# Kernel optimization log

Hardware: AMD Instinct MI355X
Metric: run time of the kernel (lower is better)

Reference implementation:

```python
import jax, jax.numpy as jnp
import numpy as np

B, T, L, D, H = 4, 8, 197, 512, 8
DK = D // H
SIM_TH = 0.0
N = T * (L - 1)  # 1568 local tokens

def _ln(x, g, b, eps=1e-5):
    x32 = x.astype(jnp.float32)
    m = jnp.mean(x32, axis=-1, keepdims=True)
    v = jnp.mean((x32 - m) ** 2, axis=-1, keepdims=True)
    return (((x32 - m) * jax.lax.rsqrt(v + eps)) * g + b).astype(x.dtype)

def _qgelu(x):
    return x * jax.nn.sigmoid(1.702 * x)

def _mha(x, w_in, b_in, w_out, b_out):
    # torch nn.MultiheadAttention, x: [S, Bt, D] (seq-first)
    S, Bt, _ = x.shape
    qkv = x @ w_in.T + b_in
    q, k, v = jnp.split(qkv, 3, axis=-1)
    q = q.reshape(S, Bt, H, DK); k = k.reshape(S, Bt, H, DK); v = v.reshape(S, Bt, H, DK)
    scores = jnp.einsum('sbhd,tbhd->bhst', q, k) / jnp.sqrt(jnp.asarray(DK, x.dtype))
    p = jax.nn.softmax(scores, axis=-1)
    o = jnp.einsum('bhst,tbhd->sbhd', p, v).reshape(S, Bt, D)
    return o @ w_out.T + b_out

def _resblock(x, ln1g, ln1b, inw, inb, outw, outb, ln2g, ln2b, fcw, fcb, pw, pb):
    x = x + _mha(_ln(x, ln1g, ln1b), inw, inb, outw, outb)
    h = _qgelu(_ln(x, ln2g, ln2b) @ fcw.T + fcb)
    return x + h @ pw.T + pb

def _build_graph(x, g_mask):
    xd = jax.lax.stop_gradient(x)  # matches x.detach()
    xn = xd / jnp.maximum(jnp.linalg.norm(xd, axis=-1, keepdims=True), 1e-12)
    sim = jnp.einsum('bnd,bmd->bnm', xn, xn)
    adj = jnp.where(sim < SIM_TH, 0.0, sim)
    return adj * g_mask  # t != 1 branch

def _graph_attn(x, mask, wq, bq, wk, bk, wv, bv, wo, bo):
    Bb, Nn, _ = x.shape
    def heads(a):
        return a.reshape(Bb, Nn, H, DK).transpose(0, 2, 1, 3)
    Q = heads(x @ wq.T + bq); K = heads(x @ wk.T + bk); V = heads(x @ wv.T + bv)
    scores = jnp.einsum('bhnd,bhmd->bhnm', Q, K) / jnp.sqrt(jnp.asarray(DK, x.dtype))
    m = mask[:, None]  # [b,1,N,N]
    scores = jnp.where(m == 0, -jnp.inf, scores * m)  # scores*mask then masked_fill(mask==0,-inf)
    p = jax.nn.softmax(scores, axis=-1)
    o = jnp.einsum('bhnm,bhmd->bhnd', p, V).transpose(0, 2, 1, 3).reshape(Bb, Nn, D)
    return o @ wo.T + bo

def _forward(x, proj_w, proj_b,
             m_ln1g, m_ln1b, m_inw, m_inb, m_outw, m_outb,
             m_ln2g, m_ln2b, m_fcw, m_fcb, m_pw, m_pb,
             g_wq, g_bq, g_wk, g_bk, g_wv, g_bv, g_wo, g_bo,
             ln1g, ln1b, a_inw, a_inb, a_outw, a_outb,
             ln2g, ln2b, fcw, fcb, pw, pb, g_mask):
    b, t, l, d = x.shape
    x = x @ proj_w.T + proj_b
    glob = x[:, :, 0, :].transpose(1, 0, 2)  # [t,b,d]
    msg = (m_ln1g, m_ln1b, m_inw, m_inb, m_outw, m_outb, m_ln2g, m_ln2b, m_fcw, m_fcb, m_pw, m_pb)
    glob = _resblock(glob, *msg)
    glob = _resblock(glob, *msg)  # message_attn applied twice (shared weights)
    glob = glob.reshape(1, t, b, d)
    loc = x[:, :, 1:, :].reshape(b, t * (l - 1), d)
    gm = _build_graph(loc, g_mask)
    loc = _graph_attn(loc, gm, g_wq, g_bq, g_wk, g_bk, g_wv, g_bv, g_wo, g_bo)
    loc = loc.reshape(b, t, l - 1, d).transpose(2, 1, 0, 3)  # [l-1,t,b,d]
    y = jnp.concatenate([glob, loc], axis=0).reshape(l, t * b, d)
    y = y + _mha(_ln(y, ln1g, ln1b), a_inw, a_inb, a_outw, a_outb)
    y = y + _qgelu(_ln(y, ln2g, ln2b) @ fcw.T + fcb) @ pw.T + pb
    return y.reshape(l, t, b, d).transpose(2, 1, 0, 3)  # [b,t,l,d]

def setup_inputs() -> dict:
    key = jax.random.key(0)
    ks = jax.random.split(key, 64)
    s = 0.02
    def w(i, shape):
        return jax.random.normal(ks[i], shape, jnp.float32) * s
    ones = jnp.ones((D,), jnp.float32); zeros = jnp.zeros((D,), jnp.float32)
    gm = (jax.random.uniform(ks[60], (N, N)) < 0.5).astype(jnp.float32)
    gm = gm.at[jnp.arange(N), jnp.arange(N)].set(1.0)  # keep self-edges so no row is fully masked
    return dict(
        x=jax.random.normal(ks[0], (B, T, L, D), jnp.float32),
        proj_w=w(1, (D, D)), proj_b=jnp.zeros((D,), jnp.float32),
        m_ln1g=ones, m_ln1b=zeros,
        m_inw=w(2, (3 * D, D)), m_inb=jnp.zeros((3 * D,), jnp.float32),
        m_outw=w(3, (D, D)), m_outb=zeros,
        m_ln2g=ones, m_ln2b=zeros,
        m_fcw=w(4, (4 * D, D)), m_fcb=jnp.zeros((4 * D,), jnp.float32),
        m_pw=w(5, (D, 4 * D)), m_pb=zeros,
        g_wq=w(6, (D, D)), g_bq=zeros, g_wk=w(7, (D, D)), g_bk=zeros,
        g_wv=w(8, (D, D)), g_bv=zeros, g_wo=w(9, (D, D)), g_bo=zeros,
        ln1g=ones, ln1b=zeros,
        a_inw=w(10, (3 * D, D)), a_inb=jnp.zeros((3 * D,), jnp.float32),
        a_outw=w(11, (D, D)), a_outb=zeros,
        ln2g=ones, ln2b=zeros,
        fcw=w(12, (4 * D, D)), fcb=jnp.zeros((4 * D,), jnp.float32),
        pw=w(13, (D, 4 * D)), pb=zeros,
        g_mask=gm,
    )

def reference(x, proj_w, proj_b, m_ln1g, m_ln1b, m_inw, m_inb, m_outw, m_outb,
              m_ln2g, m_ln2b, m_fcw, m_fcb, m_pw, m_pb,
              g_wq, g_bq, g_wk, g_bk, g_wv, g_bv, g_wo, g_bo,
              ln1g, ln1b, a_inw, a_inb, a_outw, a_outb,
              ln2g, ln2b, fcw, fcb, pw, pb, g_mask):
    return _forward(x, proj_w, proj_b, m_ln1g, m_ln1b, m_inw, m_inb, m_outw, m_outb,
                    m_ln2g, m_ln2b, m_fcw, m_fcb, m_pw, m_pb,
                    g_wq, g_bq, g_wk, g_bk, g_wv, g_bv, g_wo, g_bo,
                    ln1g, ln1b, a_inw, a_inb, a_outw, a_outb,
                    ln2g, ln2b, fcw, fcb, pw, pb, g_mask)
```

## Files before the change

### kernel.cpp

```cpp
#include <hip/hip_runtime.h>
#include <hip/hip_bf16.h>

typedef unsigned short u16;
typedef __attribute__((ext_vector_type(8))) short bf16x8;
typedef __attribute__((ext_vector_type(4))) float f32x4;

#define FINF __builtin_huge_valf()

static __device__ __forceinline__ float bf2f(u16 v){ union{unsigned u; float f;} c; c.u = ((unsigned)v)<<16; return c.f; }
static __device__ __forceinline__ u16 f2bf(float f){ union{__hip_bfloat16 h; u16 u;} c; c.h = __float2bfloat16(f); return c.u; }
static __device__ __forceinline__ bf16x8 scale8(bf16x8 v, float s){
  bf16x8 o;
  #pragma unroll
  for (int e=0;e<8;e++) o[e] = (short)f2bf(bf2f((u16)v[e])*s);
  return o;
}

static __device__ __forceinline__ void gload16(const void* g, void* l){
  __builtin_amdgcn_global_load_lds(
      (const __attribute__((address_space(1))) void*)g,
      (__attribute__((address_space(3))) void*)l, 16, 0, 0);
}

#define WAIT_VM0()   { asm volatile("s_waitcnt vmcnt(0)" ::: "memory"); __builtin_amdgcn_sched_barrier(0); }
#define BARRIER()    { __builtin_amdgcn_sched_barrier(0); __builtin_amdgcn_s_barrier(); __builtin_amdgcn_sched_barrier(0); }

struct CvtArgs {
  const float* src[14];
  u16* dst[14];
  int n[14];
};
__global__ __launch_bounds__(256) void cvt_multi(CvtArgs a){
  int seg = blockIdx.y;
  const float* s = a.src[seg]; u16* d = a.dst[seg]; int n = a.n[seg];
  for (int i = (blockIdx.x*256 + threadIdx.x)*4; i < n; i += gridDim.x*256*4){
    float4 v = *(const float4*)(s + i);
    ushort4 o = { f2bf(v.x), f2bf(v.y), f2bf(v.z), f2bf(v.w) };
    *(ushort4*)(d + i) = o;
  }
}

__global__ __launch_bounds__(256) void concat_bias(const float* a, const float* b, const float* c, float* o){
  int i = blockIdx.x*256 + threadIdx.x;
  o[i] = i < 512 ? a[i] : (i < 1024 ? b[i-512] : c[i-1024]);
}

template<int BM, int EPI>
__global__ __launch_bounds__(256,2) void gemm_nt(
    const u16* __restrict__ A, const u16* __restrict__ Bw,
    const float* __restrict__ bias, const float* aux, void* out,
    int M, int Nn, int K, int ldc, long aBatch, long bBatch, long cBatch)
{
  constexpr int MI = BM/32;
  constexpr int WSPAN = BM/2;
  __shared__ __align__(16) u16 a_lds[2*BM*64];
  __shared__ __align__(16) u16 b_lds[2*128*64];
  const int z = blockIdx.z;
  const u16* Az = A + (long)z*aBatch;
  const u16* Bz = Bw + (long)z*bBatch;
  const int n0 = blockIdx.x*128, m0 = blockIdx.y*BM;
  const int t = threadIdx.x, lane = t & 63, wave = t >> 6;
  const int wr = wave >> 1, wc = wave & 1;
  const int r = lane & 15, kq = lane >> 4;

  const int srow = t >> 3;
  const int scol = ((t&7)*8) ^ ((srow&7)<<3);
  int rowA[MI], rowB[4];
  #pragma unroll
  for (int i=0;i<MI;i++){ int ga = m0 + i*32 + srow; rowA[i] = ga < M ? ga : M-1; }
  #pragma unroll
  for (int i=0;i<4;i++){ int gb = n0 + i*32 + srow; rowB[i] = gb < Nn ? gb : Nn-1; }

  f32x4 acc[MI][4] = {};
  const int nkt = K >> 6;

  auto STAGE = [&](int kt, int buf){
    const long koff = (long)kt*64 + scol;
    #pragma unroll
    for (int i=0;i<MI;i++)
      gload16(Az + (long)rowA[i]*K + koff, (char*)a_lds + buf*(BM*128) + i*4096 + wave*1024);
    #pragma unroll
    for (int i=0;i<4;i++)
      gload16(Bz + (long)rowB[i]*K + koff, (char*)b_lds + buf*16384 + i*4096 + wave*1024);
  };

  STAGE(0,0);
  WAIT_VM0(); BARRIER();
  for (int kt=0; kt<nkt; kt++){
    const int cur = kt&1;
    if (kt+1 < nkt) STAGE(kt+1, cur^1);
    const u16* al = a_lds + cur*BM*64;
    const u16* bl = b_lds + cur*8192;
    #pragma unroll
    for (int kk=0; kk<2; kk++){
      bf16x8 af[MI], bfr[4];
      #pragma unroll
      for (int i=0;i<MI;i++){
        int rw = wr*WSPAN + i*16 + r;
        af[i] = *(const bf16x8*)&al[rw*64 + ((kk*32 + kq*8) ^ ((rw&7)<<3))];
      }
      #pragma unroll
      for (int j=0;j<4;j++){
        int rw = wc*64 + j*16 + r;
        bfr[j] = *(const bf16x8*)&bl[rw*64 + ((kk*32 + kq*8) ^ ((rw&7)<<3))];
      }
      #pragma unroll
      for (int i=0;i<MI;i++)
        #pragma unroll
        for (int j=0;j<4;j++)
          acc[i][j] = __builtin_amdgcn_mfma_f32_16x16x32_bf16(af[i], bfr[j], acc[i][j], 0,0,0);
    }
    WAIT_VM0(); BARRIER();
  }

  #pragma unroll
  for (int i=0;i<MI;i++){
    #pragma unroll
    for (int j=0;j<4;j++){
      int gcol = n0 + wc*64 + j*16 + r;
      if (gcol >= Nn) continue;
      float bv = bias ? bias[gcol] : 0.f;
      #pragma unroll
      for (int rr=0; rr<4; rr++){
        int grow = m0 + wr*WSPAN + i*16 + kq*4 + rr;
        if (grow >= M) continue;
        float v = acc[i][j][rr] + bv;
        if constexpr (EPI==0){
          ((float*)out)[(long)z*cBatch + (long)grow*ldc + gcol] = v;
        } else if constexpr (EPI==1){
          ((u16*)out)[(long)z*cBatch + (long)grow*ldc + gcol] = f2bf(v);
        } else if constexpr (EPI==2){
          long idx = (long)z*cBatch + (long)grow*ldc + gcol;
          ((float*)out)[idx] = aux[idx] + v;
        } else if constexpr (EPI==3){
          float g = v / (1.f + __expf(-1.702f*v));
          ((u16*)out)[(long)z*cBatch + (long)grow*ldc + gcol] = f2bf(g);
        } else if constexpr (EPI==4){
          float adj = v < 0.f ? 0.f : v;
          float gmv = aux[(long)grow*Nn + gcol];
          ((u16*)out)[(long)z*cBatch + (long)grow*ldc + gcol] = f2bf(adj*gmv);
        } else if constexpr (EPI==5){
          int b = grow/1568, n = grow%1568, tt = n/196, lp = n%196;
          int yrow = (1+lp)*32 + tt*4 + b;
          ((float*)out)[(long)yrow*ldc + gcol] = v;
        } else if constexpr (EPI==6){
          long idx = (long)grow*ldc + gcol;
          int l = grow>>5, rb = grow&31, tt = rb>>2, bb = rb&3;
          ((float*)out)[((long)((bb*8+tt)*197) + l)*512 + gcol] = aux[idx] + v;
        }
      }
    }
  }
}

template<bool MASKED>
__global__ __launch_bounds__(512,4) void flash_attn(
    const u16* __restrict__ QKV, const u16* __restrict__ gmask, u16* __restrict__ Out,
    int nq, int nk, long qBatch, long qRow, long oBatch, long oRow, long gmBatch)
{
  __shared__ __align__(16) u16 k_lds[2*4096];
  __shared__ __align__(16) u16 vt[64*72];
  __shared__ __align__(16) u16 p_lds[8][16*72];
  __shared__ __align__(16) u16 g_lds[MASKED ? 2*8192 : 8];
  const int t = threadIdx.x, lane = t&63, wave = t>>6;
  const int r = lane&15, kq = lane>>4;
  const int h = blockIdx.y, z = blockIdx.z;
  const u16* Qb = QKV + (long)z*qBatch + h*64;
  const u16* Kb = Qb + 512;
  const u16* Vb = Qb + 1024;
  const u16* Gz = gmask + (long)z*gmBatch;
  const int qt0 = blockIdx.x*128;
  const int q0  = qt0 + wave*16;

  bf16x8 qf0, qf1;
  { int qi = q0 + r; if (qi > nq-1) qi = nq-1;
    const u16* qp = Qb + (long)qi*qRow + kq*8;
    qf0 = scale8(*(const bf16x8*)qp, 0.125f);
    qf1 = scale8(*(const bf16x8*)(qp+32), 0.125f); }

  const int srow = t>>3;
  const int scol = ((t&7)*8) ^ ((srow&7)<<3);
  const int vcc  = (t&7)*8;

  uint4 vv;
  auto stage_k = [&](int kt, int buf){
    int j = kt*64 + srow; if (j > nk-1) j = nk-1;
    gload16(Kb + (long)j*qRow + scol, (char*)k_lds + buf*8192 + wave*1024);
  };
  auto stage_g = [&](int kt, int buf){
    #pragma unroll
    for (int i=0;i<2;i++){
      int qr = qt0 + i*64 + srow; if (qr > nq-1) qr = nq-1;
      gload16(Gz + (long)qr*nk + kt*64 + scol, (char*)g_lds + buf*16384 + i*8192 + wave*1024);
    }
  };
  auto load_v = [&](int kt){
    int vj = kt*64 + srow; if (vj > nk-1) vj = nk-1;
    vv = *(const uint4*)(Vb + (long)vj*qRow + vcc);
  };
  auto write_vt = [&](){
    #pragma unroll
    for (int e=0;e<8;e++)
      vt[(vcc+e)*72 + (srow ^ (e<<3))] = ((const u16*)&vv)[e];
  };

  bf16x8 ONES;
  #pragma unroll
  for (int e=0;e<8;e++) ONES[e] = (short)0x3F80;

  float m_[4] = {-FINF,-FINF,-FINF,-FINF};
  f32x4 o_[4] = {}; f32x4 ol = {};

  const int nkt = (nk + 63) >> 6;
  stage_k(0,0); if (MASKED) stage_g(0,0); load_v(0);
  __syncthreads();
  for (int kt=0; kt<nkt; kt++){
    const int cur = kt&1;
    write_vt();
    __syncthreads();
    if (kt+1 < nkt){
      stage_k(kt+1, cur^1);
      if (MASKED) stage_g(kt+1, cur^1);
      load_v(kt+1);
    }

    float s[4][4];
    const u16* kl = k_lds + cur*4096;
    #pragma unroll
    for (int sub=0; sub<4; sub++){
      int rw = sub*16 + r; int sw = (rw&7)<<3;
      bf16x8 kf0 = *(const bf16x8*)&kl[rw*64 + ((kq*8) ^ sw)];
      bf16x8 kf1 = *(const bf16x8*)&kl[rw*64 + ((32 + kq*8) ^ sw)];
      f32x4 sc = {};
      sc = __builtin_amdgcn_mfma_f32_16x16x32_bf16(qf0, kf0, sc, 0,0,0);
      sc = __builtin_amdgcn_mfma_f32_16x16x32_bf16(qf1, kf1, sc, 0,0,0);
      #pragma unroll
      for (int rr=0;rr<4;rr++) s[sub][rr] = sc[rr];
    }
    #pragma unroll
    for (int sub=0; sub<4; sub++){
      int key = kt*64 + sub*16 + r;
      bool kdead = key >= nk;
      #pragma unroll
      for (int rr=0;rr<4;rr++){
        float sv = s[sub][rr];
        if constexpr (MASKED){
          int lrow = wave*16 + kq*4 + rr;
          u16 g = g_lds[cur*8192 + lrow*64 + ((sub*16+r) ^ ((lrow&7)<<3))];
          if (g == 0 || kdead) sv = -FINF; else sv *= bf2f(g);
        } else {
          if (kdead) sv = -FINF;
        }
        s[sub][rr] = sv;
      }
    }
    #pragma unroll
    for (int rr=0;rr<4;rr++){
      float mx = fmaxf(fmaxf(s[0][rr],s[1][rr]), fmaxf(s[2][rr],s[3][rr]));
      #pragma unroll
      for (int d=1; d<16; d<<=1) mx = fmaxf(mx, __shfl_xor(mx, d));
      float mnew = fmaxf(m_[rr], mx);
      float fac = (m_[rr] == -FINF) ? 0.f : __expf(m_[rr] - mnew);
      #pragma unroll
      for (int sub=0;sub<4;sub++)
        s[sub][rr] = (s[sub][rr] == -FINF) ? 0.f : __expf(s[sub][rr] - mnew);
      m_[rr] = mnew;
      o_[0][rr]*=fac; o_[1][rr]*=fac; o_[2][rr]*=fac; o_[3][rr]*=fac; ol[rr]*=fac;
    }
    #pragma unroll
    for (int rr=0;rr<4;rr++){
      int prow = kq*4+rr;
      #pragma unroll
      for (int sub=0;sub<4;sub++)
        p_lds[wave][prow*72 + ((sub*16+r) ^ ((prow&7)<<3))] = f2bf(s[sub][rr]);
    }
    #pragma unroll
    for (int c=0;c<2;c++){
      bf16x8 pf = *(const bf16x8*)&p_lds[wave][r*72 + ((c*32 + kq*8) ^ ((r&7)<<3))];
      #pragma unroll
      for (int j=0;j<4;j++){
        bf16x8 vf = *(const bf16x8*)&vt[(j*16+r)*72 + ((c*32 + kq*8) ^ ((r&7)<<3))];
        o_[j] = __builtin_amdgcn_mfma_f32_16x16x32_bf16(pf, vf, o_[j], 0,0,0);
      }
      ol = __builtin_amdgcn_mfma_f32_16x16x32_bf16(pf, ONES, ol, 0,0,0);
    }
    __syncthreads();
  }

  #pragma unroll
  for (int rr=0;rr<4;rr++){
    int qrow = q0 + kq*4 + rr;
    if (qrow >= nq) continue;
    float inv = ol[rr] > 0.f ? 1.f/ol[rr] : 0.f;
    #pragma unroll
    for (int j=0;j<4;j++)
      Out[(long)z*oBatch + (long)qrow*oRow + h*64 + j*16 + r] = f2bf(o_[j][rr]*inv);
  }
}

__global__ __launch_bounds__(256) void ln_rows(const float* __restrict__ in,
    const float* __restrict__ g, const float* __restrict__ b, u16* __restrict__ out, int rows)
{
  int wave = threadIdx.x >> 6, lane = threadIdx.x & 63;
  int row = blockIdx.x*4 + wave;
  if (row >= rows) return;
  const float4* x = (const float4*)(in + (long)row*512);
  float4 v0 = x[lane], v1 = x[lane+64];
  float s  = v0.x+v0.y+v0.z+v0.w + v1.x+v1.y+v1.z+v1.w;
  float ss = v0.x*v0.x+v0.y*v0.y+v0.z*v0.z+v0.w*v0.w + v1.x*v1.x+v1.y*v1.y+v1.z*v1.z+v1.w*v1.w;
  #pragma unroll
  for (int d=1; d<64; d<<=1){ s += __shfl_xor(s,d); ss += __shfl_xor(ss,d); }
  float mean = s * (1.f/512.f);
  float var = ss * (1.f/512.f) - mean*mean;
  float rs = rsqrtf(var + 1e-5f);
  const float4* gg = (const float4*)g; const float4* bb = (const float4*)b;
  float4 g0 = gg[lane], g1 = gg[lane+64], b0 = bb[lane], b1 = bb[lane+64];
  u16* o = out + (long)row*512;
  ushort4 o0 = { f2bf((v0.x-mean)*rs*g0.x + b0.x), f2bf((v0.y-mean)*rs*g0.y + b0.y),
                 f2bf((v0.z-mean)*rs*g0.z + b0.z), f2bf((v0.w-mean)*rs*g0.w + b0.w) };
  ushort4 o1 = { f2bf((v1.x-mean)*rs*g1.x + b1.x), f2bf((v1.y-mean)*rs*g1.y + b1.y),
                 f2bf((v1.z-mean)*rs*g1.z + b1.z), f2bf((v1.w-mean)*rs*g1.w + b1.w) };
  *(ushort4*)(o + lane*4) = o0;
  *(ushort4*)(o + 256 + lane*4) = o1;
}

__global__ __launch_bounds__(256) void locprep(const float* __restrict__ y0,
    u16* __restrict__ xn, u16* __restrict__ locb)
{
  int wave = threadIdx.x >> 6, lane = threadIdx.x & 63;
  int rr = blockIdx.x*4 + wave;
  int bb = rr/1568, n = rr%1568, tt = n/196, lp = n%196;
  const float4* x = (const float4*)(y0 + ((long)((bb*8+tt)*197) + 1 + lp)*512);
  float4 v0 = x[lane], v1 = x[lane+64];
  float ss = v0.x*v0.x+v0.y*v0.y+v0.z*v0.z+v0.w*v0.w + v1.x*v1.x+v1.y*v1.y+v1.z*v1.z+v1.w*v1.w;
  #pragma unroll
  for (int d=1; d<64; d<<=1) ss += __shfl_xor(ss,d);
  float sc = 1.f / fmaxf(sqrtf(ss), 1e-12f);
  u16* ox = xn + (long)rr*512;
  u16* ol = locb + (long)rr*512;
  ushort4 a0 = { f2bf(v0.x*sc), f2bf(v0.y*sc), f2bf(v0.z*sc), f2bf(v0.w*sc) };
  ushort4 a1 = { f2bf(v1.x*sc), f2bf(v1.y*sc), f2bf(v1.z*sc), f2bf(v1.w*sc) };
  ushort4 c0 = { f2bf(v0.x), f2bf(v0.y), f2bf(v0.z), f2bf(v0.w) };
  ushort4 c1 = { f2bf(v1.x), f2bf(v1.y), f2bf(v1.z), f2bf(v1.w) };
  *(ushort4*)(ox + lane*4) = a0;  *(ushort4*)(ox + 256 + lane*4) = a1;
  *(ushort4*)(ol + lane*4) = c0;  *(ushort4*)(ol + 256 + lane*4) = c1;
}

__global__ __launch_bounds__(64) void msg_attn(const u16* __restrict__ mqkv, u16* __restrict__ matt){
  __shared__ float q_s[8][64], k_s[8][64], v_s[8][64];
  int bh = blockIdx.x; int bt = bh>>3, h = bh&7;
  int lane = threadIdx.x;
  int row = lane>>3, cc = (lane&7)*8;
  #pragma unroll
  for (int e=0;e<8;e++){
    long base = (long)(row*4 + bt)*1536 + h*64 + cc + e;
    q_s[row][cc+e] = bf2f(mqkv[base]);
    k_s[row][cc+e] = bf2f(mqkv[base + 512]);
    v_s[row][cc+e] = bf2f(mqkv[base + 1024]);
  }
  __syncthreads();
  int q = lane>>3, k = lane&7;
  float s = 0.f;
  #pragma unroll 16
  for (int d=0; d<64; d++) s += q_s[q][d]*k_s[k][d];
  s *= 0.125f;
  float mx = s;
  #pragma unroll
  for (int d=1; d<8; d<<=1) mx = fmaxf(mx, __shfl_xor(mx,d));
  float p = __expf(s - mx), ps = p;
  #pragma unroll
  for (int d=1; d<8; d<<=1) ps += __shfl_xor(ps,d);
  p /= ps;
  for (int d=0; d<64; d++){
    float ov = p * v_s[k][d];
    #pragma unroll
    for (int m=1; m<8; m<<=1) ov += __shfl_xor(ov,m);
    if (k == (d>>3)) matt[(long)(q*4 + bt)*512 + h*64 + d] = f2bf(ov);
  }
}

__global__ __launch_bounds__(256) void gather_glob(const float* __restrict__ y0, float* __restrict__ glob){
  int idx = blockIdx.x*256 + threadIdx.x;
  int orow = idx>>9, d = idx&511;
  int tt = orow>>2, bb = orow&3;
  glob[idx] = y0[((long)(bb*8+tt)*197)*512 + d];
}
__global__ __launch_bounds__(256) void copy32(const float* __restrict__ glob, float* __restrict__ y){
  int idx = blockIdx.x*256 + threadIdx.x;
  y[idx] = glob[idx];
}

extern "C" void kernel_launch(void* const* d_in, const int* in_sizes, int n_in,
                              void* d_out, int out_size, void* d_ws, size_t ws_size,
                              hipStream_t stream)
{
  const float* x      = (const float*)d_in[0];
  const float* proj_w = (const float*)d_in[1];
  const float* proj_b = (const float*)d_in[2];
  const float* m_ln1g = (const float*)d_in[3];
  const float* m_ln1b = (const float*)d_in[4];
  const float* m_inw  = (const float*)d_in[5];
  const float* m_inb  = (const float*)d_in[6];
  const float* m_outw = (const float*)d_in[7];
  const float* m_outb = (const float*)d_in[8];
  const float* m_ln2g = (const float*)d_in[9];
  const float* m_ln2b = (const float*)d_in[10];
  const float* m_fcw  = (const float*)d_in[11];
  const float* m_fcb  = (const float*)d_in[12];
  const float* m_pw   = (const float*)d_in[13];
  const float* m_pb   = (const float*)d_in[14];
  const float* g_wq = (const float*)d_in[15]; const float* g_bq = (const float*)d_in[16];
  const float* g_wk = (const float*)d_in[17]; const float* g_bk = (const float*)d_in[18];
  const float* g_wv = (const float*)d_in[19]; const float* g_bv = (const float*)d_in[20];
  const float* g_wo = (const float*)d_in[21]; const float* g_bo = (const float*)d_in[22];
  const float* ln1g = (const float*)d_in[23]; const float* ln1b = (const float*)d_in[24];
  const float* a_inw = (const float*)d_in[25]; const float* a_inb = (const float*)d_in[26];
  const float* a_outw = (const float*)d_in[27]; const float* a_outb = (const float*)d_in[28];
  const float* ln2g = (const float*)d_in[29]; const float* ln2b = (const float*)d_in[30];
  const float* fcw = (const float*)d_in[31]; const float* fcb = (const float*)d_in[32];
  const float* pw = (const float*)d_in[33]; const float* pb = (const float*)d_in[34];
  const float* g_mask = (const float*)d_in[35];

  if (ws_size < (size_t)99753984) return;

  char* ws = (char*)d_ws;
  u16* WB = (u16*)ws;
  const long WPROJ=0, WMIN=262144, WMOUT=1048576, WMFC=1310720, WMP=2359296,
             WGQ=3407872, WGK=3670016, WGV=3932160, WGO=4194304,
             WAIN=4456448, WAOUT=5242880, WFC=5505024, WP=6553600;
  float* y0   = (float*)(ws + 15204352);
  float* y    = (float*)(ws + 28114944);
  u16* lnbuf  = (u16*)(ws + 41025536);
  u16* locb   = (u16*)(ws + 47480832);
  u16* qkv    = (u16*)(ws + 53903360);
  u16* xb     = (u16*)(ws + 73269248);
  u16* gm     = (u16*)(ws + 73269248);
  u16* hbuf   = (u16*)(ws + 73269248);
  u16* obuf   = (u16*)(ws + 92938240);
  float* glob = (float*)(ws + 99393536);
  u16* mlnb   = (u16*)(ws + 99459072);
  u16* mqkv   = (u16*)(ws + 99491840);
  u16* matt   = (u16*)(ws + 99590144);
  u16* mh     = (u16*)(ws + 99622912);
  float* gbias = (float*)(ws + 99622912);

  CvtArgs ca;
  auto setseg=[&](int i, const float* s, u16* d, int n){ ca.src[i]=s; ca.dst[i]=d; ca.n[i]=n; };
  setseg(0,  x,      xb,       6304*512);
  setseg(1,  proj_w, WB+WPROJ, 262144);
  setseg(2,  m_inw,  WB+WMIN,  786432);
  setseg(3,  m_outw, WB+WMOUT, 262144);
  setseg(4,  m_fcw,  WB+WMFC,  1048576);
  setseg(5,  m_pw,   WB+WMP,   1048576);
  setseg(6,  g_wq,   WB+WGQ,   262144);
  setseg(7,  g_wk,   WB+WGK,   262144);
  setseg(8,  g_wv,   WB+WGV,   262144);
  setseg(9,  g_wo,   WB+WGO,   262144);
  setseg(10, a_inw,  WB+WAIN,  786432);
  setseg(11, a_outw, WB+WAOUT, 262144);
  setseg(12, fcw,    WB+WFC,   1048576);
  setseg(13, pw,     WB+WP,    1048576);
  cvt_multi<<<dim3(128,14), 256, 0, stream>>>(ca);

  gemm_nt<64,0><<<dim3(4,99), 256, 0, stream>>>(xb, WB+WPROJ, proj_b, nullptr, y0, 6304,512,512,512, 0,0,0);

  gather_glob<<<64,256,0,stream>>>(y0, glob);

  for (int it=0; it<2; ++it){
    ln_rows<<<8,256,0,stream>>>(glob, m_ln1g, m_ln1b, mlnb, 32);
    gemm_nt<64,1><<<dim3(12,1),256,0,stream>>>(mlnb, WB+WMIN, m_inb, nullptr, mqkv, 32,1536,512,1536, 0,0,0);
    msg_attn<<<32,64,0,stream>>>(mqkv, matt);
    gemm_nt<64,2><<<dim3(4,1),256,0,stream>>>(matt, WB+WMOUT, m_outb, glob, glob, 32,512,512,512, 0,0,0);
    ln_rows<<<8,256,0,stream>>>(glob, m_ln2g, m_ln2b, mlnb, 32);
    gemm_nt<64,3><<<dim3(16,1),256,0,stream>>>(mlnb, WB+WMFC, m_fcb, nullptr, mh, 32,2048,512,2048, 0,0,0);
    gemm_nt<64,2><<<dim3(4,1),256,0,stream>>>(mh, WB+WMP, m_pb, glob, glob, 32,512,2048,512, 0,0,0);
  }

  concat_bias<<<6,256,0,stream>>>(g_bq, g_bk, g_bv, gbias);

  locprep<<<1568,256,0,stream>>>(y0, lnbuf, locb);

  gemm_nt<128,4><<<dim3(13,13,4),256,0,stream>>>(lnbuf, lnbuf, nullptr, g_mask, gm,
      1568,1568,512,1568, 1568L*512, 1568L*512, 1568L*1568);

  gemm_nt<128,1><<<dim3(12,49),256,0,stream>>>(locb, WB+WGQ, gbias, nullptr, qkv, 6272,1536,512,1536, 0,0,0);

  flash_attn<true><<<dim3(13,8,4),512,0,stream>>>(qkv, gm, obuf,
      1568,1568, 1568L*1536, 1536, 1568L*512, 512, 1568L*1568);

  gemm_nt<64,5><<<dim3(4,98),256,0,stream>>>(obuf, WB+WGO, g_bo, nullptr, y, 6272,512,512,512, 0,0,0);

  copy32<<<64,256,0,stream>>>(glob, y);

  ln_rows<<<1576,256,0,stream>>>(y, ln1g, ln1b, lnbuf, 6304);
  gemm_nt<128,1><<<dim3(12,50),256,0,stream>>>(lnbuf, WB+WAIN, a_inb, nullptr, qkv, 6304,1536,512,1536, 0,0,0);
  flash_attn<false><<<dim3(2,8,32),512,0,stream>>>(qkv, nullptr, obuf,
      197,197, 1536, 32L*1536, 512, 32L*512, 0);
  gemm_nt<64,2><<<dim3(4,99),256,0,stream>>>(obuf, WB+WAOUT, a_outb, y, y, 6304,512,512,512, 0,0,0);

  ln_rows<<<1576,256,0,stream>>>(y, ln2g, ln2b, lnbuf, 6304);
  gemm_nt<128,3><<<dim3(16,50),256,0,stream>>>(lnbuf, WB+WFC, fcb, nullptr, hbuf, 6304,2048,512,2048, 0,0,0);
  gemm_nt<64,6><<<dim3(4,99),256,0,stream>>>(hbuf, WB+WP, pb, y, (float*)d_out, 6304,512,2048,512, 0,0,0);
}
```

Measured before the change: 612.8 us.

## Pre-transpose V globally and restructure flash attention with async V staging

New measurement: 608.0 us. No clear change (-0.8%).

```diff
diff --git a/kernel.cpp b/kernel.cpp
--- a/kernel.cpp
+++ b/kernel.cpp
@@ -45,8 +45,8 @@
   o[i] = i < 512 ? a[i] : (i < 1024 ? b[i-512] : c[i-1024]);
 }
 
-template<int BM, int EPI>
-__global__ __launch_bounds__(256,2) void gemm_nt(
+template<int BM, int EPI, int MW>
+__global__ __launch_bounds__(256,MW) void gemm_nt(
     const u16* __restrict__ A, const u16* __restrict__ Bw,
     const float* __restrict__ bias, const float* aux, void* out,
     int M, int Nn, int K, int ldc, long aBatch, long bBatch, long cBatch)
@@ -153,23 +153,68 @@
   }
 }
 
+__global__ __launch_bounds__(256) void transpose_v(
+    const u16* __restrict__ src, u16* __restrict__ vt,
+    int nrows, long zofs, long nofs, int vcol0, int outld)
+{
+  __shared__ u16 tile[64][66];
+  const int t = threadIdx.x;
+  const int nt = blockIdx.x, h = blockIdx.y, z = blockIdx.z;
+  const int n0 = nt*64;
+  const int rlo = t>>3, c0 = (t&7)*8;
+  #pragma unroll
+  for (int i=0;i<2;i++){
+    int nl = i*32 + rlo;
+    int n = n0 + nl; int nc = n < nrows ? n : nrows-1;
+    const u16* s = src + (long)z*zofs + (long)nc*nofs + vcol0 + h*64 + c0;
+    uint4 v = *(const uint4*)s;
+    bool dead = n >= nrows;
+    #pragma unroll
+    for (int e=0;e<8;e++) tile[nl][c0+e] = dead ? (u16)0 : ((const u16*)&v)[e];
+  }
+  __syncthreads();
+  #pragma unroll
+  for (int i=0;i<2;i++){
+    int d = i*32 + rlo;
+    u16 tmp[8];
+    #pragma unroll
+    for (int e=0;e<8;e++) tmp[e] = tile[c0+e][d];
+    int ncol = n0 + c0;
+    if (ncol + 8 <= outld){
+      u16* dst = vt + ((long)((z*8+h)*64 + d))*outld + ncol;
+      *(uint4*)dst = *(uint4*)tmp;
+    }
+  }
+}
+
 template<bool MASKED>
-__global__ __launch_bounds__(512,4) void flash_attn(
-    const u16* __restrict__ QKV, const u16* __restrict__ gmask, u16* __restrict__ Out,
-    int nq, int nk, long qBatch, long qRow, long oBatch, long oRow, long gmBatch)
+__global__ __launch_bounds__(256, MASKED?2:3) void flash2(
+    const u16* __restrict__ QKV, const u16* __restrict__ VT,
+    const u16* __restrict__ gmask, u16* __restrict__ Out,
+    int nq, int nk, int nqb, long qBatch, long qRow,
+    long oBatch, long oRow, long gmBatch, int vtld)
 {
   __shared__ __align__(16) u16 k_lds[2*4096];
-  __shared__ __align__(16) u16 vt[64*72];
-  __shared__ __align__(16) u16 p_lds[8][16*72];
-  __shared__ __align__(16) u16 g_lds[MASKED ? 2*8192 : 8];
+  __shared__ __align__(16) u16 v_lds[2*4096];
+  __shared__ __align__(16) u16 g_lds[MASKED ? 2*4096 : 8];
+  __shared__ __align__(16) u16 p_lds[4][16*72];
+  int h, z, qb;
+  if constexpr (MASKED){
+    int id = blockIdx.x;
+    int a = id>>6, c = id&7; h = (id>>3)&7;
+    int G = a*8 + c;
+    if (G >= 4*nqb) return;
+    z = G / nqb; qb = G % nqb;
+  } else {
+    qb = blockIdx.x; h = blockIdx.y; z = blockIdx.z;
+  }
   const int t = threadIdx.x, lane = t&63, wave = t>>6;
   const int r = lane&15, kq = lane>>4;
-  const int h = blockIdx.y, z = blockIdx.z;
   const u16* Qb = QKV + (long)z*qBatch + h*64;
   const u16* Kb = Qb + 512;
-  const u16* Vb = Qb + 1024;
-  const u16* Gz = gmask + (long)z*gmBatch;
-  const int qt0 = blockIdx.x*128;
+  const u16* Vt = VT + (long)(z*8+h)*64*vtld;
+  const u16* Gz = MASKED ? (gmask + (long)z*gmBatch) : nullptr;
+  const int qt0 = qb*64;
   const int q0  = qt0 + wave*16;
 
   bf16x8 qf0, qf1;
@@ -180,28 +225,25 @@
 
   const int srow = t>>3;
   const int scol = ((t&7)*8) ^ ((srow&7)<<3);
-  const int vcc  = (t&7)*8;
-
-  uint4 vv;
-  auto stage_k = [&](int kt, int buf){
-    int j = kt*64 + srow; if (j > nk-1) j = nk-1;
-    gload16(Kb + (long)j*qRow + scol, (char*)k_lds + buf*8192 + wave*1024);
-  };
-  auto stage_g = [&](int kt, int buf){
+
+  auto stage = [&](int kt, int buf){
     #pragma unroll
     for (int i=0;i<2;i++){
-      int qr = qt0 + i*64 + srow; if (qr > nq-1) qr = nq-1;
-      gload16(Gz + (long)qr*nk + kt*64 + scol, (char*)g_lds + buf*16384 + i*8192 + wave*1024);
-    }
-  };
-  auto load_v = [&](int kt){
-    int vj = kt*64 + srow; if (vj > nk-1) vj = nk-1;
-    vv = *(const uint4*)(Vb + (long)vj*qRow + vcc);
-  };
-  auto write_vt = [&](){
-    #pragma unroll
-    for (int e=0;e<8;e++)
-      vt[(vcc+e)*72 + (srow ^ (e<<3))] = ((const u16*)&vv)[e];
+      int j = kt*64 + i*32 + srow; if (j > nk-1) j = nk-1;
+      gload16(Kb + (long)j*qRow + scol, (char*)k_lds + buf*8192 + i*4096 + wave*1024);
+    }
+    #pragma unroll
+    for (int i=0;i<2;i++){
+      int d = i*32 + srow;
+      gload16(Vt + (long)d*vtld + kt*64 + scol, (char*)v_lds + buf*8192 + i*4096 + wave*1024);
+    }
+    if constexpr (MASKED){
+      #pragma unroll
+      for (int i=0;i<2;i++){
+        int qr = qt0 + i*32 + srow; if (qr > nq-1) qr = nq-1;
+        gload16(Gz + (long)qr*nk + kt*64 + scol, (char*)g_lds + buf*8192 + i*4096 + wave*1024);
+      }
+    }
   };
 
   bf16x8 ONES;
@@ -212,17 +254,11 @@
   f32x4 o_[4] = {}; f32x4 ol = {};
 
   const int nkt = (nk + 63) >> 6;
-  stage_k(0,0); if (MASKED) stage_g(0,0); load_v(0);
+  stage(0,0);
   __syncthreads();
   for (int kt=0; kt<nkt; kt++){
     const int cur = kt&1;
-    write_vt();
-    __syncthreads();
-    if (kt+1 < nkt){
-      stage_k(kt+1, cur^1);
-      if (MASKED) stage_g(kt+1, cur^1);
-      load_v(kt+1);
-    }
+    if (kt+1 < nkt) stage(kt+1, cur^1);
 
     float s[4][4];
     const u16* kl = k_lds + cur*4096;
@@ -246,7 +282,7 @@
         float sv = s[sub][rr];
         if constexpr (MASKED){
           int lrow = wave*16 + kq*4 + rr;
-          u16 g = g_lds[cur*8192 + lrow*64 + ((sub*16+r) ^ ((lrow&7)<<3))];
+          u16 g = g_lds[cur*4096 + lrow*64 + ((sub*16+r) ^ ((lrow&7)<<3))];
           if (g == 0 || kdead) sv = -FINF; else sv *= bf2f(g);
         } else {
           if (kdead) sv = -FINF;
@@ -274,12 +310,14 @@
       for (int sub=0;sub<4;sub++)
         p_lds[wave][prow*72 + ((sub*16+r) ^ ((prow&7)<<3))] = f2bf(s[sub][rr]);
     }
+    const u16* vl = v_lds + cur*4096;
     #pragma unroll
     for (int c=0;c<2;c++){
       bf16x8 pf = *(const bf16x8*)&p_lds[wave][r*72 + ((c*32 + kq*8) ^ ((r&7)<<3))];
       #pragma unroll
       for (int j=0;j<4;j++){
-        bf16x8 vf = *(const bf16x8*)&vt[(j*16+r)*72 + ((c*32 + kq*8) ^ ((r&7)<<3))];
+        int rw = j*16 + r;
+        bf16x8 vf = *(const bf16x8*)&vl[rw*64 + ((c*32 + kq*8) ^ ((rw&7)<<3))];
         o_[j] = __builtin_amdgcn_mfma_f32_16x16x32_bf16(pf, vf, o_[j], 0,0,0);
       }
       ol = __builtin_amdgcn_mfma_f32_16x16x32_bf16(pf, ONES, ol, 0,0,0);
@@ -431,10 +469,12 @@
   float* y0   = (float*)(ws + 15204352);
   float* y    = (float*)(ws + 28114944);
   u16* lnbuf  = (u16*)(ws + 41025536);
+  u16* vtg    = (u16*)(ws + 41025536);
   u16* locb   = (u16*)(ws + 47480832);
   u16* qkv    = (u16*)(ws + 53903360);
   u16* xb     = (u16*)(ws + 73269248);
   u16* gm     = (u16*)(ws + 73269248);
+  u16* vt2    = (u16*)(ws + 73269248);
   u16* hbuf   = (u16*)(ws + 73269248);
   u16* obuf   = (u16*)(ws + 92938240);
   float* glob = (float*)(ws + 99393536);
@@ -462,43 +502,46 @@
   setseg(13, pw,     WB+WP,    1048576);
   cvt_multi<<<dim3(128,14), 256, 0, stream>>>(ca);
 
-  gemm_nt<64,0><<<dim3(4,99), 256, 0, stream>>>(xb, WB+WPROJ, proj_b, nullptr, y0, 6304,512,512,512, 0,0,0);
+  gemm_nt<64,0,3><<<dim3(4,99), 256, 0, stream>>>(xb, WB+WPROJ, proj_b, nullptr, y0, 6304,512,512,512, 0,0,0);
 
   gather_glob<<<64,256,0,stream>>>(y0, glob);
 
   for (int it=0; it<2; ++it){
     ln_rows<<<8,256,0,stream>>>(glob, m_ln1g, m_ln1b, mlnb, 32);
-    gemm_nt<64,1><<<dim3(12,1),256,0,stream>>>(mlnb, WB+WMIN, m_inb, nullptr, mqkv, 32,1536,512,1536, 0,0,0);
+    gemm_nt<64,1,3><<<dim3(12,1),256,0,stream>>>(mlnb, WB+WMIN, m_inb, nullptr, mqkv, 32,1536,512,1536, 0,0,0);
     msg_attn<<<32,64,0,stream>>>(mqkv, matt);
-    gemm_nt<64,2><<<dim3(4,1),256,0,stream>>>(matt, WB+WMOUT, m_outb, glob, glob, 32,512,512,512, 0,0,0);
+    gemm_nt<64,2,3><<<dim3(4,1),256,0,stream>>>(matt, WB+WMOUT, m_outb, glob, glob, 32,512,512,512, 0,0,0);
     ln_rows<<<8,256,0,stream>>>(glob, m_ln2g, m_ln2b, mlnb, 32);
-    gemm_nt<64,3><<<dim3(16,1),256,0,stream>>>(mlnb, WB+WMFC, m_fcb, nullptr, mh, 32,2048,512,2048, 0,0,0);
-    gemm_nt<64,2><<<dim3(4,1),256,0,stream>>>(mh, WB+WMP, m_pb, glob, glob, 32,512,2048,512, 0,0,0);
+    gemm_nt<64,3,3><<<dim3(16,1),256,0,stream>>>(mlnb, WB+WMFC, m_fcb, nullptr, mh, 32,2048,512,2048, 0,0,0);
+    gemm_nt<64,2,3><<<dim3(4,1),256,0,stream>>>(mh, WB+WMP, m_pb, glob, glob, 32,512,2048,512, 0,0,0);
   }
 
   concat_bias<<<6,256,0,stream>>>(g_bq, g_bk, g_bv, gbias);
 
   locprep<<<1568,256,0,stream>>>(y0, lnbuf, locb);
 
-  gemm_nt<128,4><<<dim3(13,13,4),256,0,stream>>>(lnbuf, lnbuf, nullptr, g_mask, gm,
+  gemm_nt<128,4,2><<<dim3(13,13,4),256,0,stream>>>(lnbuf, lnbuf, nullptr, g_mask, gm,
       1568,1568,512,1568, 1568L*512, 1568L*512, 1568L*1568);
 
-  gemm_nt<128,1><<<dim3(12,49),256,0,stream>>>(locb, WB+WGQ, gbias, nullptr, qkv, 6272,1536,512,1536, 0,0,0);
-
-  flash_attn<true><<<dim3(13,8,4),512,0,stream>>>(qkv, gm, obuf,
-      1568,1568, 1568L*1536, 1536, 1568L*512, 512, 1568L*1568);
-
-  gemm_nt<64,5><<<dim3(4,98),256,0,stream>>>(obuf, WB+WGO, g_bo, nullptr, y, 6272,512,512,512, 0,0,0);
+  gemm_nt<128,1,2><<<dim3(12,49),256,0,stream>>>(locb, WB+WGQ, gbias, nullptr, qkv, 6272,1536,512,1536, 0,0,0);
+
+  transpose_v<<<dim3(25,8,4),256,0,stream>>>(qkv, vtg, 1568, 1568L*1536, 1536L, 1024, 1568);
+
+  flash2<true><<<832,256,0,stream>>>(qkv, vtg, gm, obuf,
+      1568,1568,25, 1568L*1536, 1536, 1568L*512, 512, 1568L*1568, 1568);
+
+  gemm_nt<64,5,3><<<dim3(4,98),256,0,stream>>>(obuf, WB+WGO, g_bo, nullptr, y, 6272,512,512,512, 0,0,0);
 
   copy32<<<64,256,0,stream>>>(glob, y);
 
   ln_rows<<<1576,256,0,stream>>>(y, ln1g, ln1b, lnbuf, 6304);
-  gemm_nt<128,1><<<dim3(12,50),256,0,stream>>>(lnbuf, WB+WAIN, a_inb, nullptr, qkv, 6304,1536,512,1536, 0,0,0);
-  flash_attn<false><<<dim3(2,8,32),512,0,stream>>>(qkv, nullptr, obuf,
-      197,197, 1536, 32L*1536, 512, 32L*512, 0);
-  gemm_nt<64,2><<<dim3(4,99),256,0,stream>>>(obuf, WB+WAOUT, a_outb, y, y, 6304,512,512,512, 0,0,0);
+  gemm_nt<128,1,2><<<dim3(12,50),256,0,stream>>>(lnbuf, WB+WAIN, a_inb, nullptr, qkv, 6304,1536,512,1536, 0,0,0);
+  transpose_v<<<dim3(4,8,32),256,0,stream>>>(qkv, vt2, 197, 1536L, 32L*1536, 1024, 256);
+  flash2<false><<<dim3(4,8,32),256,0,stream>>>(qkv, vt2, nullptr, obuf,
+      197,197,4, 1536, 32L*1536, 512, 32L*512, 0, 256);
+  gemm_nt<64,2,3><<<dim3(4,99),256,0,stream>>>(obuf, WB+WAOUT, a_outb, y, y, 6304,512,512,512, 0,0,0);
 
   ln_rows<<<1576,256,0,stream>>>(y, ln2g, ln2b, lnbuf, 6304);
-  gemm_nt<128,3><<<dim3(16,50),256,0,stream>>>(lnbuf, WB+WFC, fcb, nullptr, hbuf, 6304,2048,512,2048, 0,0,0);
-  gemm_nt<64,6><<<dim3(4,99),256,0,stream>>>(hbuf, WB+WP, pb, y, (float*)d_out, 6304,512,2048,512, 0,0,0);
-}
+  gemm_nt<128,3,2><<<dim3(16,50),256,0,stream>>>(lnbuf, WB+WFC, fcb, nullptr, hbuf, 6304,2048,512,2048, 0,0,0);
+  gemm_nt<64,6,3><<<dim3(4,99),256,0,stream>>>(hbuf, WB+WP, pb, y, (float*)d_out, 6304,512,2048,512, 0,0,0);
+}
```
